# Kernel optimization log

Measured on AMD Instinct MI355X. Metric: run time of the kernel, lower is better.

## Reference

```python
import jax, jax.numpy as jnp
import numpy as np

B, N, M, DIM, H, DH = 2, 1024, 32, 128, 8, 16
DI = H * DH          # dim_inner = 128
S = 5                # sum of (1, max_degree, max_degree), max_degree = 2
DMLP = 256           # int(2.0 * dim_inner)
EPS = 1e-5
CLAMP = 50.0

def _ln(x, w):
    mu = x.mean(-1, keepdims=True)
    var = ((x - mu) ** 2).mean(-1, keepdims=True)
    return (x - mu) / jnp.sqrt(var + EPS) * w

def _split_heads(t):
    t = t.reshape(*t.shape[:-1], H, DH)
    return jnp.moveaxis(t, -2, 1)

def _gather(t, idx):
    # t: (b, h, n, ...), idx: (b, n, m) -> (b, h, n, m, ...)
    return jax.vmap(lambda tb, ib: tb[:, ib])(t, idx)

def setup_inputs():
    key = jax.random.key(0)
    ks = jax.random.split(key, 30)
    nrm = lambda i, shp, s=1.0: jax.random.normal(ks[i], shp, jnp.float32) * s
    return dict(
        h=nrm(0, (B, N, DIM)),
        t_ij=nrm(1, (B, N, M, DIM)),
        r_ij_1=nrm(2, (B, N, M, 3)),
        r_ij_2=nrm(3, (B, N, M, 5)),
        x_1=nrm(4, (B, N, DIM, 3)),
        x_2=nrm(5, (B, N, DIM, 5)),
        neighbor_indices=jax.random.randint(ks[6], (B, N, M), 0, N),
        neighbor_mask=jnp.ones((B, N, M), dtype=bool),
        ln_i_w=jnp.ones((DIM,)),
        ln_j_w=jnp.ones((DIM,)),
        Wq=nrm(7, (DIM, DI), DIM ** -0.5),
        Wk=nrm(8, (DIM, DI), DIM ** -0.5),
        Wv1=nrm(9, (DIM, DMLP), DIM ** -0.5), bv1=jnp.zeros((DMLP,)),
        Wv2=nrm(10, (DMLP, S * DI), DMLP ** -0.5), bv2=jnp.zeros((S * DI,)),
        Wpv1=nrm(11, (DIM, DMLP), DIM ** -0.5), bpv1=jnp.zeros((DMLP,)),
        Wpv2=nrm(12, (DMLP, S * DI), DMLP ** -0.5), bpv2=jnp.zeros((S * DI,)),
        Wek=nrm(13, (DIM, S * DI), DIM ** -0.5),
        Wev=nrm(14, (DIM, S * DI), DIM ** -0.5),
        Wg=nrm(15, (DIM, H * S), DIM ** -0.5), bg=jnp.zeros((H * S,)),
        Wo=nrm(16, (DI, DIM), DI ** -0.5),
    )

def reference(h, t_ij, r_ij_1, r_ij_2, x_1, x_2, neighbor_indices, neighbor_mask,
              ln_i_w, ln_j_w, Wq, Wk, Wv1, bv1, Wv2, bv2, Wpv1, bpv1, Wpv2, bpv2,
              Wek, Wev, Wg, bg, Wo):
    hi = _ln(h, ln_i_w)
    hj = _ln(h, ln_j_w)
    q = _split_heads(hi @ Wq)                                                   # (b,h,n,dh)
    k = _split_heads(hj @ Wk)                                                   # (b,h,n,dh)
    v = _split_heads((jax.nn.silu(hj @ Wv1 + bv1) @ Wv2 + bv2).reshape(B, N, S, DI))       # (b,h,n,s,dh)
    pv = _split_heads((jax.nn.silu(hj @ Wpv1 + bpv1) @ Wpv2 + bpv2).reshape(B, N, S, DI))  # (b,h,n,s,dh)
    ek = _split_heads(jax.nn.silu(t_ij @ Wek).reshape(B, N, M, S, DI))          # (b,h,i,j,s,dh)
    ev = _split_heads((t_ij @ Wev).reshape(B, N, M, S, DI))                     # (b,h,i,j,s,dh)

    idx = neighbor_indices
    k_n = _gather(k, idx)                                                        # (b,h,i,j,dh)
    v_n = _gather(v, idx)                                                        # (b,h,i,j,s,dh)
    pv_n = _gather(pv, idx)                                                      # (b,h,i,j,s,dh)

    keys = k_n[..., None, :] * ek                                                # (b,h,i,j,s,dh)
    sim = jnp.einsum('bhid,bhijsd->bhijs', q, keys)
    sim = jnp.tanh(sim / CLAMP) * CLAMP
    neg = -jnp.finfo(sim.dtype).max
    sim = jnp.where(neighbor_mask[:, None, :, :, None], sim, neg)
    attn = jax.nn.softmax(sim, axis=-2)                                          # softmax over neighbors j

    sea = attn[..., None] * v_n + ev * pv_n                                      # (b,h,i,j,s,dh)
    gates = jax.nn.sigmoid(hi @ Wg + bg).reshape(B, N, H, S)
    gates = jnp.moveaxis(gates, 2, 1)[:, :, :, None, :, None]                    # (b,h,i,1,s,1)
    out = sea * gates
    out = jnp.moveaxis(out, 1, -2).reshape(B, N, M, S, DI)                       # merge heads
    out = out @ Wo                                                               # (b,i,j,s,dim)

    h_res = out[:, :, :, 0, :].sum(axis=2)                                       # (b,i,dim)
    r_sc1, r_sc2 = out[:, :, :, 1, :], out[:, :, :, 2, :]
    x_sc1, x_sc2 = out[:, :, :, 3, :], out[:, :, :, 4, :]

    def deg_residual(r_ij_l, x_l, r_sc, x_sc):
        r_res = jnp.einsum('bijm,bijd->bidm', r_ij_l, r_sc)
        x_nbr = jax.vmap(lambda xb, ib: xb[ib])(x_l, idx)                        # (b,i,j,d,m)
        x_res = jnp.einsum('bijdm,bijd->bidm', x_nbr, x_sc)
        return r_res + x_res

    x_res_1 = deg_residual(r_ij_1, x_1, r_sc1, x_sc1)
    x_res_2 = deg_residual(r_ij_2, x_2, r_sc2, x_sc2)
    return (h_res, x_res_1, x_res_2)
```

## Files before the change

### kernel.cpp

```cpp
#include <hip/hip_runtime.h>
#include <hip/hip_bf16.h>
#include <math.h>

#define BB    2
#define NPTS  1024
#define MM    32
#define DIMM  128
#define HH    8
#define DHH   16
#define SS    5
#define DMLPC 256
#define SDI   640
#define NNODE (BB*NPTS)
#define NN128 (NNODE*DIMM)

typedef __attribute__((ext_vector_type(8))) short bf16x8;
typedef __attribute__((ext_vector_type(4))) float f32x4;
typedef __attribute__((ext_vector_type(4))) float fvec4;

__device__ __forceinline__ float frcp(float x){ return __builtin_amdgcn_rcpf(x); }
__device__ __forceinline__ float sigf(float x){ return frcp(1.0f+__expf(-x)); }
__device__ __forceinline__ float siluf(float x){ return x*frcp(1.0f+__expf(-x)); }
__device__ __forceinline__ unsigned short f2bf(float x){
  unsigned u = __float_as_uint(x);
  u += 0x7fffu + ((u>>16)&1u);
  return (unsigned short)(u>>16);
}
__device__ __forceinline__ float bfu2f(unsigned short u){ return __uint_as_float(((unsigned)u)<<16); }

#define SWZT 76544
#define T4C  2097152
__global__ __launch_bounds__(256) void prep_kernel(
    const float* __restrict__ Wq,  const float* __restrict__ Wk,
    const float* __restrict__ Wv1, const float* __restrict__ Wpv1,
    const float* __restrict__ Wv2, const float* __restrict__ Wpv2,
    const float* __restrict__ Wek, const float* __restrict__ Wev,
    const float* __restrict__ Wo,  const float* __restrict__ Wg,
    const float* __restrict__ t_ij, const float* __restrict__ x1g,
    const float* __restrict__ x2g,
    unsigned short* __restrict__ wsw, unsigned short* __restrict__ tb,
    unsigned short* __restrict__ x1p, unsigned short* __restrict__ x2p)
{
  int i = blockIdx.x*256 + threadIdx.x;
  if (i < SWZT){
    int f = i >> 6, lane = i & 63;
    const float* W; int ncols, nkt, fb;
    if      (f <   32){ W=Wq;   ncols=128; nkt=4; fb=0;    }
    else if (f <   64){ W=Wk;   ncols=128; nkt=4; fb=32;   }
    else if (f <  128){ W=Wv1;  ncols=256; nkt=4; fb=64;   }
    else if (f <  192){ W=Wpv1; ncols=256; nkt=4; fb=128;  }
    else if (f <  512){ W=Wv2;  ncols=640; nkt=8; fb=192;  }
    else if (f <  832){ W=Wpv2; ncols=640; nkt=8; fb=512;  }
    else if (f <  992){ W=Wek;  ncols=640; nkt=4; fb=832;  }
    else if (f < 1152){ W=Wev;  ncols=640; nkt=4; fb=992;  }
    else if (f < 1184){ W=Wo;   ncols=128; nkt=4; fb=1152; }
    else              { W=Wg;   ncols=40;  nkt=4; fb=1184; }
    int fl = f - fb;
    int kt = fl % nkt, nt = fl / nkt;
    int row = kt*32 + ((lane>>4)*8);
    int col = nt*16 + (lane&15);
    unsigned px[4];
    if (col < ncols){
      #pragma unroll
      for (int e2=0; e2<4; ++e2){
        unsigned lo = f2bf(W[(size_t)(row+2*e2  )*ncols + col]);
        unsigned hi = f2bf(W[(size_t)(row+2*e2+1)*ncols + col]);
        px[e2] = lo | (hi<<16);
      }
    } else {
      px[0]=px[1]=px[2]=px[3]=0u;
    }
    ((uint4*)wsw)[(size_t)f*64 + lane] = make_uint4(px[0],px[1],px[2],px[3]);
  } else if (i < SWZT + T4C){
    int q = i - SWZT;
    fvec4 v = __builtin_nontemporal_load((const fvec4*)t_ij + q);
    unsigned a = (unsigned)f2bf(v[0]) | ((unsigned)f2bf(v[1])<<16);
    unsigned b = (unsigned)f2bf(v[2]) | ((unsigned)f2bf(v[3])<<16);
    unsigned long long pv = (unsigned long long)a | ((unsigned long long)b << 32);
    __builtin_nontemporal_store(pv, (unsigned long long*)tb + q);
  } else if (i < SWZT + T4C + NN128){
    int nc = i - (SWZT + T4C);
    const float* sp = x1g + (size_t)nc*3;
    unsigned long long pk = (unsigned long long)f2bf(sp[0])
                          | ((unsigned long long)f2bf(sp[1])<<16)
                          | ((unsigned long long)f2bf(sp[2])<<32);
    __builtin_nontemporal_store(pk, (unsigned long long*)(x1p + (size_t)nc*4));
  } else {
    int nc = i - (SWZT + T4C + NN128);
    const float* sp = x2g + (size_t)nc*5;
    unsigned long long lo = (unsigned long long)f2bf(sp[0])
                          | ((unsigned long long)f2bf(sp[1])<<16)
                          | ((unsigned long long)f2bf(sp[2])<<32)
                          | ((unsigned long long)f2bf(sp[3])<<48);
    unsigned long long hi = (unsigned long long)f2bf(sp[4]);
    __builtin_nontemporal_store(lo, (unsigned long long*)(x2p + (size_t)nc*8));
    __builtin_nontemporal_store(hi, (unsigned long long*)(x2p + (size_t)nc*8 + 4));
  }
}

__global__ __launch_bounds__(256) void node_kernel(
    const float* __restrict__ h,
    const float* __restrict__ lniw, const float* __restrict__ lnjw,
    const unsigned short* __restrict__ wsw,
    const float* __restrict__ bv1, const float* __restrict__ bpv1,
    const float* __restrict__ bv2, const float* __restrict__ bpv2,
    const float* __restrict__ bg,
    unsigned short* __restrict__ qb, unsigned short* __restrict__ kb,
    unsigned short* __restrict__ vpvb, float* __restrict__ go)
{
  const int br  = blockIdx.x & 1;
  const int n0  = (blockIdx.x >> 1) * 16;
  const int tid = threadIdx.x;
  const int wid = tid>>6, lane = tid&63;
  const int u   = lane&15;

  const unsigned short* wqk_sw = wsw + (br ? 16384 : 0);
  const unsigned short* w1_sw  = wsw + (br ? 65536 : 32768);
  const unsigned short* w2_sw  = wsw + (br ? 262144 : 98304);
  const unsigned short* wg_sw  = wsw + 606208;
  const float* b1 = br ? bpv1 : bv1;
  const float* b2 = br ? bpv2 : bv2;

  __shared__ unsigned short hib[16][132], hjb[16][132];
  __shared__ unsigned short m1[16][260];

  {
    const int row = tid>>4, cg = tid&15;
    const float* hp = h + (size_t)(n0+row)*DIMM + cg*8;
    fvec4 p0 = *(const fvec4*)hp;
    fvec4 p1 = *(const fvec4*)(hp+4);
    float x[8] = {p0[0],p0[1],p0[2],p0[3],p1[0],p1[1],p1[2],p1[3]};
    float s1=0.f, s2=0.f;
    #pragma unroll
    for (int e=0;e<8;++e){ s1+=x[e]; s2+=x[e]*x[e]; }
    #pragma unroll
    for (int m=1;m<16;m<<=1){ s1+=__shfl_xor(s1,m); s2+=__shfl_xor(s2,m); }
    const float mu = s1*(1.f/DIMM), ms = s2*(1.f/DIMM);
    const float rstd = rsqrtf(ms-mu*mu+1e-5f);
    #pragma unroll
    for (int e=0;e<8;++e){
      float xn = (x[e]-mu)*rstd;
      int c = cg*8+e;
      hib[row][c] = f2bf(xn*lniw[c]);
      hjb[row][c] = f2bf(xn*lnjw[c]);
    }
  }
  __syncthreads();

  bf16x8 aj[4];
  #pragma unroll
  for (int kt=0;kt<4;++kt) aj[kt] = *(const bf16x8*)&hjb[u][kt*32+(lane>>4)*8];

  {
    bf16x8 afr[4];
    if (br == 0){
      #pragma unroll
      for (int kt=0;kt<4;++kt) afr[kt] = *(const bf16x8*)&hib[u][kt*32+(lane>>4)*8];
    } else {
      #pragma unroll
      for (int kt=0;kt<4;++kt) afr[kt] = aj[kt];
    }
    unsigned short* outb = br ? kb : qb;
    const bf16x8* bfp = (const bf16x8*)wqk_sw;
    for (int i2=0;i2<2;++i2){
      const int nt = wid*2+i2;
      f32x4 acc = {0.f,0.f,0.f,0.f};
      #pragma unroll
      for (int kt=0;kt<4;++kt)
        acc = __builtin_amdgcn_mfma_f32_16x16x32_bf16(afr[kt], bfp[(size_t)(nt*4+kt)*64+lane], acc, 0,0,0);
      #pragma unroll
      for (int r=0;r<4;++r)
        outb[(size_t)(n0+(lane>>4)*4+r)*DIMM + nt*16+u] = f2bf(acc[r]);
    }
  }

  {
    const bf16x8* bfp = (const bf16x8*)w1_sw;
    for (int i2=0;i2<4;++i2){
      const int nt = wid*4+i2;
      f32x4 acc = {0.f,0.f,0.f,0.f};
      #pragma unroll
      for (int kt=0;kt<4;++kt)
        acc = __builtin_amdgcn_mfma_f32_16x16x32_bf16(aj[kt], bfp[(size_t)(nt*4+kt)*64+lane], acc, 0,0,0);
      const float bv = b1[nt*16+u];
      #pragma unroll
      for (int r=0;r<4;++r)
        m1[(lane>>4)*4+r][nt*16+u] = f2bf(siluf(acc[r]+bv));
    }
  }
  __syncthreads();

  {
    bf16x8 am[8];
    #pragma unroll
    for (int kt=0;kt<8;++kt) am[kt] = *(const bf16x8*)&m1[u][kt*32+(lane>>4)*8];
    const bf16x8* bfp = (const bf16x8*)w2_sw;
    for (int i2=0;i2<10;++i2){
      const int nt = wid*10+i2;
      f32x4 acc = {0.f,0.f,0.f,0.f};
      #pragma unroll
      for (int kt=0;kt<8;++kt)
        acc = __builtin_amdgcn_mfma_f32_16x16x32_bf16(am[kt], bfp[(size_t)(nt*8+kt)*64+lane], acc, 0,0,0);
      const int c = nt*16+u, s = c>>7, d = c&127;
      const float bb = b2[c];
      #pragma unroll
      for (int r=0;r<4;++r)
        vpvb[(size_t)(n0+(lane>>4)*4+r)*(SS*256) + s*256 + d*2 + br] = f2bf(acc[r]+bb);
    }
  }

  if (br == 0 && wid == 0){
    bf16x8 ai[4];
    #pragma unroll
    for (int kt=0;kt<4;++kt) ai[kt] = *(const bf16x8*)&hib[u][kt*32+(lane>>4)*8];
    const bf16x8* bfp = (const bf16x8*)wg_sw;
    #pragma unroll
    for (int nt=0;nt<3;++nt){
      f32x4 acc = {0.f,0.f,0.f,0.f};
      #pragma unroll
      for (int kt=0;kt<4;++kt)
        acc = __builtin_amdgcn_mfma_f32_16x16x32_bf16(ai[kt], bfp[(size_t)(nt*4+kt)*64+lane], acc, 0,0,0);
      const int col = nt*16+u;
      if (col < HH*SS){
        const float bb = bg[col];
        #pragma unroll
        for (int r=0;r<4;++r)
          go[(size_t)(n0+(lane>>4)*4+r)*(HH*SS) + col] = sigf(acc[r]+bb);
      }
    }
  }
}

__global__ __launch_bounds__(256) void edge_kernel(
    const unsigned short* __restrict__ tb,
    const float* __restrict__ r1g, const float* __restrict__ r2g,
    const unsigned short* __restrict__ x1p, const unsigned short* __restrict__ x2p,
    const int*  __restrict__ nbr,
    const unsigned short* __restrict__ wsw,
    const unsigned short* __restrict__ qb, const unsigned short* __restrict__ kb,
    const unsigned short* __restrict__ vpvb,
    const float* __restrict__ go,
    float* __restrict__ out,
    float* __restrict__ p1, float* __restrict__ p2,
    float* __restrict__ p3, float* __restrict__ p4,
    int use_atomic)
{
  const int bid = blockIdx.x;
  const int xcd = bid & 7, wslot = bid >> 3;
  const int nid = xcd*256 + (wslot & 255);
  const int s   = wslot >> 8;
  const int b0  = nid >> 10;
  const int tid = threadIdx.x;
  const int wid = tid >> 6, lane = tid & 63;
  const int u   = lane & 15;

  const bf16x8* wekf = (const bf16x8*)(wsw + 425984);
  const bf16x8* wevf = (const bf16x8*)(wsw + 507904);
  const bf16x8* wof  = (const bf16x8*)(wsw + 589824);

  __shared__ unsigned short kn_lds[MM][132];
  __shared__ unsigned short sea_lds[MM][132];
  __shared__ float          sim_s[HH][33];
  __shared__ float          g_s[HH];
  __shared__ float          r_s[MM][5];

  bf16x8 afr[2][4];
  {
    const unsigned short* tp = tb + (size_t)nid*MM*DIMM;
    #pragma unroll
    for (int mt=0; mt<2; ++mt)
      #pragma unroll
      for (int kt=0; kt<4; ++kt)
        afr[mt][kt] = *(const bf16x8*)&tp[(mt*16+u)*DIMM + kt*32 + (lane>>4)*8];
  }

  #pragma unroll
  for (int it=0; it<4; ++it){
    int e = tid + it*256;
    int j = e>>5, d = (e&31)*4;
    int nj = nbr[nid*MM + j];
    *(uint2*)&kn_lds[j][d] = *(const uint2*)&kb[(unsigned)(b0*NPTS + nj)*DIMM + d];
  }
  int njr[2][4];
  #pragma unroll
  for (int mt=0; mt<2; ++mt)
    #pragma unroll
    for (int r=0; r<4; ++r)
      njr[mt][r] = nbr[nid*MM + mt*16 + (lane>>4)*4 + r];
  if (tid < HH) g_s[tid] = go[nid*HH*SS + tid*SS + s];
  if (s == 1){ for (int e=tid; e<MM*3; e+=256) r_s[e/3][e%3] = r1g[(size_t)nid*MM*3 + e]; }
  if (s == 2){ for (int e=tid; e<MM*5; e+=256) r_s[e/5][e%5] = r2g[(size_t)nid*MM*5 + e]; }
  const float ql = bfu2f(qb[(unsigned)nid*DIMM + wid*16 + u]);
  const float qh = bfu2f(qb[(unsigned)nid*DIMM + (wid+4)*16 + u]);
  const unsigned* vpvu = (const unsigned*)vpvb;
  unsigned vp[2][2][4];
  #pragma unroll
  for (int hl=0; hl<2; ++hl){
    const int col = (wid*2+hl)*16 + u;
    #pragma unroll
    for (int mt=0; mt<2; ++mt)
      #pragma unroll
      for (int r=0; r<4; ++r)
        vp[hl][mt][r] = vpvu[(unsigned)(b0*NPTS + njr[mt][r])*(SS*DIMM) + s*DIMM + col];
  }
  __syncthreads();

  #pragma unroll
  for (int i=0; i<2; ++i){
    const int hh = wid + 4*i;
    const int nt = s*8 + hh;
    const float qv = i ? qh : ql;
    f32x4 acc0 = {0.f,0.f,0.f,0.f}, acc1 = {0.f,0.f,0.f,0.f};
    #pragma unroll
    for (int kt=0; kt<4; ++kt){
      bf16x8 bfr = wekf[(size_t)(nt*4+kt)*64 + lane];
      acc0 = __builtin_amdgcn_mfma_f32_16x16x32_bf16(afr[0][kt], bfr, acc0, 0,0,0);
      acc1 = __builtin_amdgcn_mfma_f32_16x16x32_bf16(afr[1][kt], bfr, acc1, 0,0,0);
    }
    #pragma unroll
    for (int mt=0; mt<2; ++mt){
      #pragma unroll
      for (int r=0; r<4; ++r){
        int j = mt*16 + (lane>>4)*4 + r;
        float val = (mt==0) ? acc0[r] : acc1[r];
        float p = siluf(val) * qv * bfu2f(kn_lds[j][hh*16 + u]);
        p += __shfl_xor(p,1); p += __shfl_xor(p,2);
        p += __shfl_xor(p,4); p += __shfl_xor(p,8);
        if (u == 0) sim_s[hh][j] = p;
      }
    }
  }
  __syncthreads();

  {
    const int hh = tid >> 5, j = tid & 31;
    float praw = sim_s[hh][j];
    float v = 50.f - 100.f*frcp(__expf(praw*0.04f) + 1.f);
    float mx = v;
    #pragma unroll
    for (int m=1; m<32; m<<=1) mx = fmaxf(mx, __shfl_xor(mx,m));
    float e = __expf(v - mx);
    float sum = e;
    #pragma unroll
    for (int m=1; m<32; m<<=1) sum += __shfl_xor(sum,m);
    sim_s[hh][j] = g_s[hh] * e * frcp(sum);
  }
  __syncthreads();

  #pragma unroll
  for (int hl=0; hl<2; ++hl){
    const int hh = wid*2 + hl;
    const int nt = s*8 + hh;
    const int col = hh*16 + u;
    const float gp = g_s[hh];
    f32x4 acc0 = {0.f,0.f,0.f,0.f}, acc1 = {0.f,0.f,0.f,0.f};
    #pragma unroll
    for (int kt=0; kt<4; ++kt){
      bf16x8 bfr = wevf[(size_t)(nt*4+kt)*64 + lane];
      acc0 = __builtin_amdgcn_mfma_f32_16x16x32_bf16(afr[0][kt], bfr, acc0, 0,0,0);
      acc1 = __builtin_amdgcn_mfma_f32_16x16x32_bf16(afr[1][kt], bfr, acc1, 0,0,0);
    }
    #pragma unroll
    for (int mt=0; mt<2; ++mt){
      #pragma unroll
      for (int r=0; r<4; ++r){
        int j = mt*16 + (lane>>4)*4 + r;
        float evv = (mt==0) ? acc0[r] : acc1[r];
        unsigned w = vp[hl][mt][r];
        float vn  = bfu2f((unsigned short)(w & 0xffffu));
        float pvn = bfu2f((unsigned short)(w >> 16));
        float sea = sim_s[hh][j]*vn + gp*evv*pvn;
        sea_lds[j][col] = f2bf(sea);
      }
    }
  }
  __syncthreads();

  float hres[2] = {0.f,0.f};
  float xr1[2][3] = {{0.f,0.f,0.f},{0.f,0.f,0.f}};
  float xr2[2][5] = {{0.f,0.f,0.f,0.f,0.f},{0.f,0.f,0.f,0.f,0.f}};
  #pragma unroll
  for (int ntl=0; ntl<2; ++ntl){
    const int col = (wid*2+ntl)*16 + u;
    #pragma unroll
    for (int mt=0; mt<2; ++mt){
      f32x4 acc = {0.f,0.f,0.f,0.f};
      #pragma unroll
      for (int kt=0; kt<4; ++kt){
        bf16x8 a = *(const bf16x8*)&sea_lds[mt*16 + u][kt*32 + (lane>>4)*8];
        bf16x8 wfr = wof[(size_t)((wid*2+ntl)*4+kt)*64 + lane];
        acc = __builtin_amdgcn_mfma_f32_16x16x32_bf16(a, wfr, acc, 0,0,0);
      }
      #pragma unroll
      for (int r=0; r<4; ++r){
        int j = mt*16 + (lane>>4)*4 + r;
        float ov = acc[r];
        if (s == 0){
          hres[ntl] += ov;
        } else if (s == 1){
          #pragma unroll
          for (int m=0;m<3;++m) xr1[ntl][m] += r_s[j][m]*ov;
        } else if (s == 2){
          #pragma unroll
          for (int m=0;m<5;++m) xr2[ntl][m] += r_s[j][m]*ov;
        } else if (s == 3){
          unsigned idx = (unsigned)(b0*NPTS + njr[mt][r])*DIMM + col;
          uint2 w2 = *(const uint2*)&x1p[(size_t)idx*4];
          xr1[ntl][0] += bfu2f((unsigned short)(w2.x & 0xffffu))*ov;
          xr1[ntl][1] += bfu2f((unsigned short)(w2.x >> 16))*ov;
          xr1[ntl][2] += bfu2f((unsigned short)(w2.y & 0xffffu))*ov;
        } else {
          unsigned idx = (unsigned)(b0*NPTS + njr[mt][r])*DIMM + col;
          uint4 w4 = *(const uint4*)&x2p[(size_t)idx*8];
          xr2[ntl][0] += bfu2f((unsigned short)(w4.x & 0xffffu))*ov;
          xr2[ntl][1] += bfu2f((unsigned short)(w4.x >> 16))*ov;
          xr2[ntl][2] += bfu2f((unsigned short)(w4.y & 0xffffu))*ov;
          xr2[ntl][3] += bfu2f((unsigned short)(w4.y >> 16))*ov;
          xr2[ntl][4] += bfu2f((unsigned short)(w4.z & 0xffffu))*ov;
        }
      }
    }
  }

  #pragma unroll
  for (int ntl=0; ntl<2; ++ntl){
    hres[ntl] += __shfl_xor(hres[ntl],16); hres[ntl] += __shfl_xor(hres[ntl],32);
    #pragma unroll
    for (int m=0;m<3;++m){ xr1[ntl][m] += __shfl_xor(xr1[ntl][m],16); xr1[ntl][m] += __shfl_xor(xr1[ntl][m],32); }
    #pragma unroll
    for (int m=0;m<5;++m){ xr2[ntl][m] += __shfl_xor(xr2[ntl][m],16); xr2[ntl][m] += __shfl_xor(xr2[ntl][m],32); }
  }
  if (lane < 16){
    const size_t b1 = (size_t)NNODE*DIMM;
    const size_t b2 = b1 + (size_t)NNODE*DIMM*3;
    #pragma unroll
    for (int ntl=0; ntl<2; ++ntl){
      int col = (wid*2+ntl)*16 + lane;
      size_t nc = (size_t)nid*DIMM + col;
      if (s == 0){
        __builtin_nontemporal_store(hres[ntl], &out[nc]);
      } else if (use_atomic){
        if (s == 1 || s == 3){
          #pragma unroll
          for (int m=0;m<3;++m) atomicAdd(&out[b1 + nc*3 + m], xr1[ntl][m]);
        } else {
          #pragma unroll
          for (int m=0;m<5;++m) atomicAdd(&out[b2 + nc*5 + m], xr2[ntl][m]);
        }
      } else {
        if (s == 1){      for (int m=0;m<3;++m) p1[nc*3+m] = xr1[ntl][m]; }
        else if (s == 2){ for (int m=0;m<5;++m) p2[nc*5+m] = xr2[ntl][m]; }
        else if (s == 3){ for (int m=0;m<3;++m) p3[nc*3+m] = xr1[ntl][m]; }
        else {            for (int m=0;m<5;++m) p4[nc*5+m] = xr2[ntl][m]; }
      }
    }
  }
}

__global__ __launch_bounds__(256) void combine_kernel(
    const float* __restrict__ p1, const float* __restrict__ p2,
    const float* __restrict__ p3, const float* __restrict__ p4,
    float* __restrict__ out)
{
  const int N1 = NNODE*DIMM*3/4;
  int i = blockIdx.x*256 + threadIdx.x;
  if (i < N1){
    fvec4 a = ((const fvec4*)p1)[i];
    fvec4 b = ((const fvec4*)p3)[i];
    ((fvec4*)(out + NNODE*DIMM))[i] = a + b;
  } else {
    int q = i - N1;
    fvec4 a = ((const fvec4*)p2)[q];
    fvec4 b = ((const fvec4*)p4)[q];
    ((fvec4*)(out + NNODE*DIMM*4))[q] = a + b;
  }
}

extern "C" void kernel_launch(void* const* d_in, const int* in_sizes, int n_in,
                              void* d_out, int out_size, void* d_ws, size_t ws_size,
                              hipStream_t stream) {
  const float* h    = (const float*)d_in[0];
  const float* t_ij = (const float*)d_in[1];
  const float* r1g  = (const float*)d_in[2];
  const float* r2g  = (const float*)d_in[3];
  const float* x1g  = (const float*)d_in[4];
  const float* x2g  = (const float*)d_in[5];
  const int*   nbr  = (const int*)d_in[6];
  const float* lniw = (const float*)d_in[8];
  const float* lnjw = (const float*)d_in[9];
  const float* Wq   = (const float*)d_in[10];
  const float* Wk   = (const float*)d_in[11];
  const float* Wv1  = (const float*)d_in[12];
  const float* bv1  = (const float*)d_in[13];
  const float* Wv2  = (const float*)d_in[14];
  const float* bv2  = (const float*)d_in[15];
  const float* Wpv1 = (const float*)d_in[16];
  const float* bpv1 = (const float*)d_in[17];
  const float* Wpv2 = (const float*)d_in[18];
  const float* bpv2 = (const float*)d_in[19];
  const float* Wek  = (const float*)d_in[20];
  const float* Wev  = (const float*)d_in[21];
  const float* Wg   = (const float*)d_in[22];
  const float* bg   = (const float*)d_in[23];
  const float* Wo   = (const float*)d_in[24];

  char* w = (char*)d_ws;
  #define CARVE(ty, name, count) ty* name = (ty*)w; w += (((size_t)(count))*sizeof(ty) + 255) & ~(size_t)255;
  CARVE(unsigned short, qb,   (size_t)NNODE*DIMM)
  CARVE(unsigned short, kb,   (size_t)NNODE*DIMM)
  CARVE(unsigned short, vpvb, (size_t)NNODE*SS*256)
  CARVE(float,          go,   (size_t)NNODE*HH*SS)
  CARVE(unsigned short, x1p,  (size_t)NN128*4)
  CARVE(unsigned short, x2p,  (size_t)NN128*8)
  CARVE(unsigned short, tb,   (size_t)NNODE*MM*DIMM)
  CARVE(unsigned short, wsw,  (size_t)1196*512)
  CARVE(float, p1, (size_t)NN128*3)
  CARVE(float, p2, (size_t)NN128*5)
  CARVE(float, p3, (size_t)NN128*3)
  CARVE(float, p4, (size_t)NN128*5)
  #undef CARVE
  int use_atomic = ((size_t)(w - (char*)d_ws) > ws_size) ? 1 : 0;

  float* outp = (float*)d_out;

  if (use_atomic){
    hipError_t _e = hipMemsetAsync(outp + (size_t)NNODE*DIMM, 0,
                                   (size_t)NNODE*DIMM*8*sizeof(float), stream);
    (void)_e;
  }

  prep_kernel<<<10539, 256, 0, stream>>>(Wq, Wk, Wv1, Wpv1, Wv2, Wpv2,
      Wek, Wev, Wo, Wg, t_ij, x1g, x2g, wsw, tb, x1p, x2p);

  node_kernel<<<NNODE/16*2, 256, 0, stream>>>(h, lniw, lnjw, wsw,
      bv1, bpv1, bv2, bpv2, bg, qb, kb, vpvb, go);

  edge_kernel<<<NNODE*SS, 256, 0, stream>>>(tb, r1g, r2g, x1p, x2p, nbr,
      wsw, qb, kb, vpvb, go, outp, p1, p2, p3, p4, use_atomic);

  if (!use_atomic){
    combine_kernel<<<2048, 256, 0, stream>>>(p1, p2, p3, p4, outp);
  }
}
```

Before: 181.5 us.

## Fuse per-head sim, softmax and sea computation in registers, dropping LDS staging

Restructures the edge attention kernel so each wave handles the same heads for the key-similarity MFMA, the softmax and the value/edge combination. The gathered keys, gates and softmax values now stay in registers, with the softmax reduced across the wave by shuffles. This removes the kn/sim/g shared-memory buffers and two block-wide barriers. In exchange, neighbor key loads become scalar per-column gathers rather than vectorized LDS staging, and register pressure rises.

```diff
diff --git a/kernel.cpp b/kernel.cpp
--- a/kernel.cpp
+++ b/kernel.cpp
@@ -253,15 +253,13 @@
   const int tid = threadIdx.x;
   const int wid = tid >> 6, lane = tid & 63;
   const int u   = lane & 15;
+  const int g4  = (lane >> 4) * 4;
 
   const bf16x8* wekf = (const bf16x8*)(wsw + 425984);
   const bf16x8* wevf = (const bf16x8*)(wsw + 507904);
   const bf16x8* wof  = (const bf16x8*)(wsw + 589824);
 
-  __shared__ unsigned short kn_lds[MM][132];
   __shared__ unsigned short sea_lds[MM][132];
-  __shared__ float          sim_s[HH][33];
-  __shared__ float          g_s[HH];
   __shared__ float          r_s[MM][5];
 
   bf16x8 afr[2][4];
@@ -271,45 +269,43 @@
     for (int mt=0; mt<2; ++mt)
       #pragma unroll
       for (int kt=0; kt<4; ++kt)
-        afr[mt][kt] = *(const bf16x8*)&tp[(mt*16+u)*DIMM + kt*32 + (lane>>4)*8];
-  }
-
-  #pragma unroll
-  for (int it=0; it<4; ++it){
-    int e = tid + it*256;
-    int j = e>>5, d = (e&31)*4;
-    int nj = nbr[nid*MM + j];
-    *(uint2*)&kn_lds[j][d] = *(const uint2*)&kb[(unsigned)(b0*NPTS + nj)*DIMM + d];
-  }
+        afr[mt][kt] = *(const bf16x8*)&tp[(mt*16+u)*DIMM + kt*32 + g4*2];
+  }
+
   int njr[2][4];
   #pragma unroll
   for (int mt=0; mt<2; ++mt)
     #pragma unroll
     for (int r=0; r<4; ++r)
-      njr[mt][r] = nbr[nid*MM + mt*16 + (lane>>4)*4 + r];
-  if (tid < HH) g_s[tid] = go[nid*HH*SS + tid*SS + s];
+      njr[mt][r] = nbr[nid*MM + mt*16 + g4 + r];
+
+  const float ql = bfu2f(qb[(unsigned)nid*DIMM + wid*16 + u]);
+  const float qh = bfu2f(qb[(unsigned)nid*DIMM + (wid+4)*16 + u]);
+
   if (s == 1){ for (int e=tid; e<MM*3; e+=256) r_s[e/3][e%3] = r1g[(size_t)nid*MM*3 + e]; }
   if (s == 2){ for (int e=tid; e<MM*5; e+=256) r_s[e/5][e%5] = r2g[(size_t)nid*MM*5 + e]; }
-  const float ql = bfu2f(qb[(unsigned)nid*DIMM + wid*16 + u]);
-  const float qh = bfu2f(qb[(unsigned)nid*DIMM + (wid+4)*16 + u]);
+
   const unsigned* vpvu = (const unsigned*)vpvb;
-  unsigned vp[2][2][4];
-  #pragma unroll
-  for (int hl=0; hl<2; ++hl){
-    const int col = (wid*2+hl)*16 + u;
-    #pragma unroll
-    for (int mt=0; mt<2; ++mt)
-      #pragma unroll
-      for (int r=0; r<4; ++r)
-        vp[hl][mt][r] = vpvu[(unsigned)(b0*NPTS + njr[mt][r])*(SS*DIMM) + s*DIMM + col];
-  }
-  __syncthreads();
 
   #pragma unroll
   for (int i=0; i<2; ++i){
     const int hh = wid + 4*i;
     const int nt = s*8 + hh;
+    const int col = hh*16 + u;
     const float qv = i ? qh : ql;
+    const float gp = go[(unsigned)nid*HH*SS + hh*SS + s];
+
+    float knv[2][4];
+    unsigned vp[2][4];
+    #pragma unroll
+    for (int mt=0; mt<2; ++mt)
+      #pragma unroll
+      for (int r=0; r<4; ++r){
+        unsigned nodej = (unsigned)(b0*NPTS + njr[mt][r]);
+        knv[mt][r] = bfu2f(kb[nodej*DIMM + col]);
+        vp[mt][r]  = vpvu[nodej*(SS*DIMM) + s*DIMM + col];
+      }
+
     f32x4 acc0 = {0.f,0.f,0.f,0.f}, acc1 = {0.f,0.f,0.f,0.f};
     #pragma unroll
     for (int kt=0; kt<4; ++kt){
@@ -317,60 +313,55 @@
       acc0 = __builtin_amdgcn_mfma_f32_16x16x32_bf16(afr[0][kt], bfr, acc0, 0,0,0);
       acc1 = __builtin_amdgcn_mfma_f32_16x16x32_bf16(afr[1][kt], bfr, acc1, 0,0,0);
     }
+
+    float v[2][4];
     #pragma unroll
     for (int mt=0; mt<2; ++mt){
       #pragma unroll
       for (int r=0; r<4; ++r){
-        int j = mt*16 + (lane>>4)*4 + r;
         float val = (mt==0) ? acc0[r] : acc1[r];
-        float p = siluf(val) * qv * bfu2f(kn_lds[j][hh*16 + u]);
+        float p = siluf(val) * qv * knv[mt][r];
         p += __shfl_xor(p,1); p += __shfl_xor(p,2);
         p += __shfl_xor(p,4); p += __shfl_xor(p,8);
-        if (u == 0) sim_s[hh][j] = p;
-      }
-    }
-  }
-  __syncthreads();
-
-  {
-    const int hh = tid >> 5, j = tid & 31;
-    float praw = sim_s[hh][j];
-    float v = 50.f - 100.f*frcp(__expf(praw*0.04f) + 1.f);
-    float mx = v;
-    #pragma unroll
-    for (int m=1; m<32; m<<=1) mx = fmaxf(mx, __shfl_xor(mx,m));
-    float e = __expf(v - mx);
-    float sum = e;
-    #pragma unroll
-    for (int m=1; m<32; m<<=1) sum += __shfl_xor(sum,m);
-    sim_s[hh][j] = g_s[hh] * e * frcp(sum);
-  }
-  __syncthreads();
-
-  #pragma unroll
-  for (int hl=0; hl<2; ++hl){
-    const int hh = wid*2 + hl;
-    const int nt = s*8 + hh;
-    const int col = hh*16 + u;
-    const float gp = g_s[hh];
-    f32x4 acc0 = {0.f,0.f,0.f,0.f}, acc1 = {0.f,0.f,0.f,0.f};
+        v[mt][r] = 50.f - 100.f*frcp(__expf(p*0.04f) + 1.f);
+      }
+    }
+
+    float mx = v[0][0];
+    #pragma unroll
+    for (int mt=0; mt<2; ++mt)
+      #pragma unroll
+      for (int r=0; r<4; ++r) mx = fmaxf(mx, v[mt][r]);
+    mx = fmaxf(mx, __shfl_xor(mx,16));
+    mx = fmaxf(mx, __shfl_xor(mx,32));
+    float ev_[2][4];
+    float sum = 0.f;
+    #pragma unroll
+    for (int mt=0; mt<2; ++mt)
+      #pragma unroll
+      for (int r=0; r<4; ++r){ ev_[mt][r] = __expf(v[mt][r]-mx); sum += ev_[mt][r]; }
+    sum += __shfl_xor(sum,16);
+    sum += __shfl_xor(sum,32);
+    const float inv = gp * frcp(sum);
+
+    f32x4 bcc0 = {0.f,0.f,0.f,0.f}, bcc1 = {0.f,0.f,0.f,0.f};
     #pragma unroll
     for (int kt=0; kt<4; ++kt){
       bf16x8 bfr = wevf[(size_t)(nt*4+kt)*64 + lane];
-      acc0 = __builtin_amdgcn_mfma_f32_16x16x32_bf16(afr[0][kt], bfr, acc0, 0,0,0);
-      acc1 = __builtin_amdgcn_mfma_f32_16x16x32_bf16(afr[1][kt], bfr, acc1, 0,0,0);
-    }
+      bcc0 = __builtin_amdgcn_mfma_f32_16x16x32_bf16(afr[0][kt], bfr, bcc0, 0,0,0);
+      bcc1 = __builtin_amdgcn_mfma_f32_16x16x32_bf16(afr[1][kt], bfr, bcc1, 0,0,0);
+    }
+
     #pragma unroll
     for (int mt=0; mt<2; ++mt){
       #pragma unroll
       for (int r=0; r<4; ++r){
-        int j = mt*16 + (lane>>4)*4 + r;
-        float evv = (mt==0) ? acc0[r] : acc1[r];
-        unsigned w = vp[hl][mt][r];
+        float evv = (mt==0) ? bcc0[r] : bcc1[r];
+        unsigned w = vp[mt][r];
         float vn  = bfu2f((unsigned short)(w & 0xffffu));
         float pvn = bfu2f((unsigned short)(w >> 16));
-        float sea = sim_s[hh][j]*vn + gp*evv*pvn;
-        sea_lds[j][col] = f2bf(sea);
+        float sea = ev_[mt][r]*inv*vn + gp*evv*pvn;
+        sea_lds[mt*16 + g4 + r][col] = f2bf(sea);
       }
     }
   }
@@ -387,13 +378,13 @@
       f32x4 acc = {0.f,0.f,0.f,0.f};
       #pragma unroll
       for (int kt=0; kt<4; ++kt){
-        bf16x8 a = *(const bf16x8*)&sea_lds[mt*16 + u][kt*32 + (lane>>4)*8];
+        bf16x8 a = *(const bf16x8*)&sea_lds[mt*16 + u][kt*32 + g4*2];
         bf16x8 wfr = wof[(size_t)((wid*2+ntl)*4+kt)*64 + lane];
         acc = __builtin_amdgcn_mfma_f32_16x16x32_bf16(a, wfr, acc, 0,0,0);
       }
       #pragma unroll
       for (int r=0; r<4; ++r){
-        int j = mt*16 + (lane>>4)*4 + r;
+        int j = mt*16 + g4 + r;
         float ov = acc[r];
         if (s == 0){
           hres[ntl] += ov;
```

Measured after the change: 186.9 us. 1.03x slower.

## Reduce over neighbors before Wo projection for slots 0-2; drop softmax max

Applied to the files above, without the earlier changes.

For slots 0, 1 and 2 the weights applied after the output projection (a plain sum over neighbors, or r_ij moments) do not depend on the projected column, so the kernel now forms those moments of sea first and then runs one small 16-row MFMA against Wo instead of a 32-row projection per neighbor. Rows of the LDS tile beyond the moment count are zeroed beforehand. It also removes the max-subtraction in the softmax, which is safe because the clamped logits stay within ±50. The cost is extra branching, and the moments are rounded to bf16 before the projection, which may change numerics slightly.

```diff
diff --git a/kernel.cpp b/kernel.cpp
--- a/kernel.cpp
+++ b/kernel.cpp
@@ -253,6 +253,8 @@
   const int tid = threadIdx.x;
   const int wid = tid >> 6, lane = tid & 63;
   const int u   = lane & 15;
+  const int g4  = (lane >> 4) * 4;
+  const int NM  = (s==0) ? 1 : ((s==1||s==3) ? 3 : 5);
 
   const bf16x8* wekf = (const bf16x8*)(wsw + 425984);
   const bf16x8* wevf = (const bf16x8*)(wsw + 507904);
@@ -286,10 +288,16 @@
   for (int mt=0; mt<2; ++mt)
     #pragma unroll
     for (int r=0; r<4; ++r)
-      njr[mt][r] = nbr[nid*MM + mt*16 + (lane>>4)*4 + r];
+      njr[mt][r] = nbr[nid*MM + mt*16 + g4 + r];
   if (tid < HH) g_s[tid] = go[nid*HH*SS + tid*SS + s];
   if (s == 1){ for (int e=tid; e<MM*3; e+=256) r_s[e/3][e%3] = r1g[(size_t)nid*MM*3 + e]; }
   if (s == 2){ for (int e=tid; e<MM*5; e+=256) r_s[e/5][e%5] = r2g[(size_t)nid*MM*5 + e]; }
+  if (s < 3){
+    for (int e=tid; e<(16-NM)*32; e+=256){
+      int row = NM + (e>>5), c4 = (e&31)*4;
+      *(uint2*)&sea_lds[row][c4] = make_uint2(0u,0u);
+    }
+  }
   const float ql = bfu2f(qb[(unsigned)nid*DIMM + wid*16 + u]);
   const float qh = bfu2f(qb[(unsigned)nid*DIMM + (wid+4)*16 + u]);
   const unsigned* vpvu = (const unsigned*)vpvb;
@@ -321,7 +329,7 @@
     for (int mt=0; mt<2; ++mt){
       #pragma unroll
       for (int r=0; r<4; ++r){
-        int j = mt*16 + (lane>>4)*4 + r;
+        int j = mt*16 + g4 + r;
         float val = (mt==0) ? acc0[r] : acc1[r];
         float p = siluf(val) * qv * bfu2f(kn_lds[j][hh*16 + u]);
         p += __shfl_xor(p,1); p += __shfl_xor(p,2);
@@ -336,10 +344,7 @@
     const int hh = tid >> 5, j = tid & 31;
     float praw = sim_s[hh][j];
     float v = 50.f - 100.f*frcp(__expf(praw*0.04f) + 1.f);
-    float mx = v;
-    #pragma unroll
-    for (int m=1; m<32; m<<=1) mx = fmaxf(mx, __shfl_xor(mx,m));
-    float e = __expf(v - mx);
+    float e = __expf(v);
     float sum = e;
     #pragma unroll
     for (int m=1; m<32; m<<=1) sum += __shfl_xor(sum,m);
@@ -360,23 +365,83 @@
       acc0 = __builtin_amdgcn_mfma_f32_16x16x32_bf16(afr[0][kt], bfr, acc0, 0,0,0);
       acc1 = __builtin_amdgcn_mfma_f32_16x16x32_bf16(afr[1][kt], bfr, acc1, 0,0,0);
     }
-    #pragma unroll
-    for (int mt=0; mt<2; ++mt){
+    if (s >= 3){
+      #pragma unroll
+      for (int mt=0; mt<2; ++mt){
+        #pragma unroll
+        for (int r=0; r<4; ++r){
+          int j = mt*16 + g4 + r;
+          float evv = (mt==0) ? acc0[r] : acc1[r];
+          unsigned w = vp[hl][mt][r];
+          float vn  = bfu2f((unsigned short)(w & 0xffffu));
+          float pvn = bfu2f((unsigned short)(w >> 16));
+          float sea = sim_s[hh][j]*vn + gp*evv*pvn;
+          sea_lds[j][col] = f2bf(sea);
+        }
+      }
+    } else {
+      float mom[5] = {0.f,0.f,0.f,0.f,0.f};
+      #pragma unroll
+      for (int mt=0; mt<2; ++mt){
+        #pragma unroll
+        for (int r=0; r<4; ++r){
+          int j = mt*16 + g4 + r;
+          float evv = (mt==0) ? acc0[r] : acc1[r];
+          unsigned w = vp[hl][mt][r];
+          float vn  = bfu2f((unsigned short)(w & 0xffffu));
+          float pvn = bfu2f((unsigned short)(w >> 16));
+          float sea = sim_s[hh][j]*vn + gp*evv*pvn;
+          if (s == 0){
+            mom[0] += sea;
+          } else {
+            for (int m=0; m<NM; ++m) mom[m] += r_s[j][m]*sea;
+          }
+        }
+      }
+      for (int m=0; m<NM; ++m){
+        mom[m] += __shfl_xor(mom[m],16);
+        mom[m] += __shfl_xor(mom[m],32);
+      }
+      if (lane < 16){
+        for (int m=0; m<NM; ++m) sea_lds[m][col] = f2bf(mom[m]);
+      }
+    }
+  }
+  __syncthreads();
+
+  if (s < 3){
+    const size_t b1 = (size_t)NNODE*DIMM;
+    #pragma unroll
+    for (int ntl=0; ntl<2; ++ntl){
+      const int nt = wid*2 + ntl;
+      f32x4 acc = {0.f,0.f,0.f,0.f};
+      #pragma unroll
+      for (int kt=0; kt<4; ++kt){
+        bf16x8 a = *(const bf16x8*)&sea_lds[u][kt*32 + (lane>>4)*8];
+        bf16x8 wfr = wof[(size_t)(nt*4+kt)*64 + lane];
+        acc = __builtin_amdgcn_mfma_f32_16x16x32_bf16(a, wfr, acc, 0,0,0);
+      }
+      const int colo = nt*16 + u;
+      const size_t nc = (size_t)nid*DIMM + colo;
       #pragma unroll
       for (int r=0; r<4; ++r){
-        int j = mt*16 + (lane>>4)*4 + r;
-        float evv = (mt==0) ? acc0[r] : acc1[r];
-        unsigned w = vp[hl][mt][r];
-        float vn  = bfu2f((unsigned short)(w & 0xffffu));
-        float pvn = bfu2f((unsigned short)(w >> 16));
-        float sea = sim_s[hh][j]*vn + gp*evv*pvn;
-        sea_lds[j][col] = f2bf(sea);
-      }
-    }
-  }
-  __syncthreads();
-
-  float hres[2] = {0.f,0.f};
+        const int m = g4 + r;
+        if (m < NM){
+          if (s == 0){
+            __builtin_nontemporal_store(acc[r], &out[nc]);
+          } else if (s == 1){
+            if (use_atomic) atomicAdd(&out[b1 + nc*3 + m], acc[r]);
+            else            p1[nc*3 + m] = acc[r];
+          } else {
+            if (use_atomic) atomicAdd(&out[b1 + (size_t)NNODE*DIMM*3 + nc*5 + m], acc[r]);
+            else            p2[nc*5 + m] = acc[r];
+          }
+        }
+      }
+    }
+    return;
+  }
+
   float xr1[2][3] = {{0.f,0.f,0.f},{0.f,0.f,0.f}};
   float xr2[2][5] = {{0.f,0.f,0.f,0.f,0.f},{0.f,0.f,0.f,0.f,0.f}};
   #pragma unroll
@@ -393,17 +458,8 @@
       }
       #pragma unroll
       for (int r=0; r<4; ++r){
-        int j = mt*16 + (lane>>4)*4 + r;
         float ov = acc[r];
-        if (s == 0){
-          hres[ntl] += ov;
-        } else if (s == 1){
-          #pragma unroll
-          for (int m=0;m<3;++m) xr1[ntl][m] += r_s[j][m]*ov;
-        } else if (s == 2){
-          #pragma unroll
-          for (int m=0;m<5;++m) xr2[ntl][m] += r_s[j][m]*ov;
-        } else if (s == 3){
+        if (s == 3){
           unsigned idx = (unsigned)(b0*NPTS + njr[mt][r])*DIMM + col;
           uint2 w2 = *(const uint2*)&x1p[(size_t)idx*4];
           xr1[ntl][0] += bfu2f((unsigned short)(w2.x & 0xffffu))*ov;
@@ -424,7 +480,6 @@
 
   #pragma unroll
   for (int ntl=0; ntl<2; ++ntl){
-    hres[ntl] += __shfl_xor(hres[ntl],16); hres[ntl] += __shfl_xor(hres[ntl],32);
     #pragma unroll
     for (int m=0;m<3;++m){ xr1[ntl][m] += __shfl_xor(xr1[ntl][m],16); xr1[ntl][m] += __shfl_xor(xr1[ntl][m],32); }
     #pragma unroll
@@ -437,10 +492,8 @@
     for (int ntl=0; ntl<2; ++ntl){
       int col = (wid*2+ntl)*16 + lane;
       size_t nc = (size_t)nid*DIMM + col;
-      if (s == 0){
-        __builtin_nontemporal_store(hres[ntl], &out[nc]);
-      } else if (use_atomic){
-        if (s == 1 || s == 3){
+      if (use_atomic){
+        if (s == 3){
           #pragma unroll
           for (int m=0;m<3;++m) atomicAdd(&out[b1 + nc*3 + m], xr1[ntl][m]);
         } else {
@@ -448,10 +501,8 @@
           for (int m=0;m<5;++m) atomicAdd(&out[b2 + nc*5 + m], xr2[ntl][m]);
         }
       } else {
-        if (s == 1){      for (int m=0;m<3;++m) p1[nc*3+m] = xr1[ntl][m]; }
-        else if (s == 2){ for (int m=0;m<5;++m) p2[nc*5+m] = xr2[ntl][m]; }
-        else if (s == 3){ for (int m=0;m<3;++m) p3[nc*3+m] = xr1[ntl][m]; }
-        else {            for (int m=0;m<5;++m) p4[nc*5+m] = xr2[ntl][m]; }
+        if (s == 3){ for (int m=0;m<3;++m) p3[nc*3+m] = xr1[ntl][m]; }
+        else {       for (int m=0;m<5;++m) p4[nc*5+m] = xr2[ntl][m]; }
       }
     }
   }
```

Result: slower. 189.9 us (+4.6%).
